# Performance work log

Hardware: AMD Instinct MI355X
Metric: run time of the kernel (lower is better)

## Reference

```python
import jax, jax.numpy as jnp
import numpy as np

B, P, M, C = 8192, 8, 2048, 1024


def setup_inputs() -> dict:
    key = jax.random.key(0)
    k1, k2 = jax.random.split(key)
    stdv = 1.0 / np.sqrt(C)
    inp = jax.random.normal(k1, (B, C), dtype=jnp.float32)
    weight = jax.random.uniform(k2, (P, M, C), dtype=jnp.float32, minval=-stdv, maxval=stdv)
    return {"input": inp, "weight": weight}


def reference(input, weight):
    # scores: [B, P, M] = <input_c, weight_pmc>
    att = jnp.einsum('bc,pmc->bpm', input, weight)
    att = jax.nn.softmax(att, axis=2)
    # combine with the same memory bank as values: [B, P, C]
    out = jnp.einsum('bpm,pmc->bpc', att, weight)
    return out
```

## Files before the change

### kernel.cpp

```cpp
#include <hip/hip_runtime.h>
#include <hip/hip_bf16.h>
#include <cstdint>
#include <cstddef>

#define B_SZ 8192
#define P_SZ 8
#define M_SZ 2048
#define C_SZ 1024

using bfrag = __attribute__((ext_vector_type(8))) short;
using facc  = __attribute__((ext_vector_type(4))) float;
using u16x4 = __attribute__((ext_vector_type(4))) unsigned short;

typedef __attribute__((address_space(1))) const void g_void;
typedef __attribute__((address_space(3))) void l_void;

__device__ __forceinline__ unsigned short f2bf(float x) {
    union { __hip_bfloat16 h; unsigned short u; } cv;
    cv.h = __float2bfloat16(x);
    return cv.u;
}
__device__ __forceinline__ float bf2f(unsigned short u) {
    union { unsigned int i; float f; } cv;
    cv.i = ((unsigned int)u) << 16;
    return cv.f;
}

#define WAIT_LGKM0() do { asm volatile("s_waitcnt lgkmcnt(0)" ::: "memory"); \
                          __builtin_amdgcn_sched_barrier(0); } while (0)
#define WAIT_VM(n)   do { asm volatile("s_waitcnt vmcnt(" #n ")" ::: "memory"); \
                          __builtin_amdgcn_sched_barrier(0); } while (0)
#define S_BARRIER()     asm volatile("s_barrier" ::: "memory")
#define LGKM0_BARRIER() asm volatile("s_waitcnt lgkmcnt(0)\n\ts_barrier" ::: "memory")
#define WAIT_VM_RAW(n)  asm volatile("s_waitcnt vmcnt(" #n ")" ::: "memory")

__global__ void cvt_q_kernel(const float* __restrict__ in, unsigned short* __restrict__ q) {
    const size_t i = (size_t)blockIdx.x * blockDim.x + threadIdx.x;
    const float4 v = ((const float4*)in)[i];
    u16x4 o = { f2bf(v.x), f2bf(v.y), f2bf(v.z), f2bf(v.w) };
    ((u16x4*)q)[i] = o;
}

__global__ void cvt_w_kernel(const float* __restrict__ w,
                             unsigned short* __restrict__ wb,
                             unsigned short* __restrict__ wt) {
    __shared__ float t[32][33];
    const int bid = blockIdx.x;
    const int p  = bid >> 11;
    const int m0 = ((bid >> 5) & 63) << 5;
    const int c0 = (bid & 31) << 5;
    const int tx = threadIdx.x & 7;
    const int ty = threadIdx.x >> 3;
    const float4 v = *(const float4*)(w + ((size_t)p*M_SZ + m0 + ty)*C_SZ + c0 + tx*4);
    u16x4 o = { f2bf(v.x), f2bf(v.y), f2bf(v.z), f2bf(v.w) };
    *(u16x4*)(wb + ((size_t)p*M_SZ + m0 + ty)*C_SZ + c0 + tx*4) = o;
    t[ty][tx*4+0] = v.x; t[ty][tx*4+1] = v.y; t[ty][tx*4+2] = v.z; t[ty][tx*4+3] = v.w;
    __syncthreads();
    float4 u2;
    u2.x = t[tx*4+0][ty]; u2.y = t[tx*4+1][ty]; u2.z = t[tx*4+2][ty]; u2.w = t[tx*4+3][ty];
    u16x4 o2 = { f2bf(u2.x), f2bf(u2.y), f2bf(u2.z), f2bf(u2.w) };
    *(u16x4*)(wt + ((size_t)p*C_SZ + c0 + ty)*M_SZ + m0 + tx*4) = o2;
}

constexpr int GLDS = 131072;

template<int KLEN>
__device__ __forceinline__ void stage_half8(const unsigned short* panelBase, char* ldsOp,
                                            int hh, int kt, int tid) {
    #pragma unroll
    for (int i = 0; i < 2; ++i) {
        const int o  = i*8192 + tid*16;
        const int rl = o >> 7;
        const int r  = hh*128 + rl;
        const int ps = (o >> 4) & 7;
        const int ls = ps ^ (r & 7);
        const unsigned short* src = panelBase + (size_t)r*KLEN + kt*64 + ls*8;
        char* dst = ldsOp + hh*16384 + i*8192 + ((tid >> 6) << 10);
        __builtin_amdgcn_global_load_lds((g_void*)src, (l_void*)dst, 16, 0, 0);
    }
}

__device__ __forceinline__ void loadA8(const char* ldsAbuf, int qm, int wm, int l15, int g,
                                       bfrag (&aF)[4][2]) {
    #pragma unroll
    for (int mf = 0; mf < 4; ++mf) {
        const int r = qm*128 + wm*64 + mf*16 + l15;
        const char* rp = ldsAbuf + r*128;
        #pragma unroll
        for (int ks = 0; ks < 2; ++ks)
            aF[mf][ks] = *(const bfrag*)(rp + (((ks*4 + g) ^ (r & 7)) << 4));
    }
}

__device__ __forceinline__ void loadB8(const char* ldsBbuf, int qn, int wn, int l15, int g,
                                       bfrag (&bF)[2][2]) {
    #pragma unroll
    for (int nf = 0; nf < 2; ++nf) {
        const int r = qn*128 + wn*32 + nf*16 + l15;
        const char* rp = ldsBbuf + r*128;
        #pragma unroll
        for (int ks = 0; ks < 2; ++ks)
            bF[nf][ks] = *(const bfrag*)(rp + (((ks*4 + g) ^ (r & 7)) << 4));
    }
}

template<int QM, int QN, int MODE, int DOSUM>
__device__ __forceinline__ void mfma_phase(const bfrag (&aF)[4][2], const bfrag (&bF)[2][2],
                                           facc (&acc)[8][4], float (&rs)[8]) {
    __builtin_amdgcn_s_setprio(1);
    #pragma unroll
    for (int ks = 0; ks < 2; ++ks)
        #pragma unroll
        for (int mf = 0; mf < 4; ++mf)
            #pragma unroll
            for (int nf = 0; nf < 2; ++nf)
                acc[QM*4 + mf][QN*2 + nf] = __builtin_amdgcn_mfma_f32_16x16x32_bf16(
                    aF[mf][ks], bF[nf][ks], acc[QM*4 + mf][QN*2 + nf], 0, 0, 0);
    if (MODE == 1 && DOSUM) {
        #pragma unroll
        for (int mf = 0; mf < 4; ++mf)
            #pragma unroll
            for (int ks = 0; ks < 2; ++ks)
                #pragma unroll
                for (int e = 0; e < 8; ++e)
                    rs[QM*4 + mf] += bf2f((unsigned short)aF[mf][ks][e]);
    }
    __builtin_amdgcn_s_setprio(0);
}

template<int KLEN, int NTN, int MODE>
__global__ __launch_bounds__(512, 2)
void gemm8(const unsigned short* __restrict__ A,
           const unsigned short* __restrict__ Bm,
           unsigned short* __restrict__ Pout,
           float* __restrict__ Oout,
           size_t APS, size_t BPS)
{
    extern __shared__ char lds[];
    const int tid  = threadIdx.x;
    const int lane = tid & 63;
    const int wid  = tid >> 6;
    const int wm   = wid >> 2;
    const int wn   = wid & 3;
    const int g    = lane >> 4;
    const int l15  = lane & 15;

    const int p       = blockIdx.x & 7;
    const int logical = blockIdx.x >> 3;
    const int nt      = logical % NTN;
    const int mt      = logical / NTN;

    const unsigned short* Abase = A  + (size_t)p*APS + (size_t)mt*256*KLEN;
    const unsigned short* Bbase = Bm + (size_t)p*BPS + (size_t)nt*256*KLEN;

    facc acc[8][4];
    #pragma unroll
    for (int i = 0; i < 8; ++i)
        #pragma unroll
        for (int j = 0; j < 4; ++j) acc[i][j] = facc{0.f, 0.f, 0.f, 0.f};
    float rs[8] = {0.f,0.f,0.f,0.f,0.f,0.f,0.f,0.f};

    constexpr int NKT = KLEN / 64;

    stage_half8<KLEN>(Bbase, lds + 32768,         0, 0, tid);
    stage_half8<KLEN>(Abase, lds + 0,             0, 0, tid);
    stage_half8<KLEN>(Bbase, lds + 32768,         1, 0, tid);
    stage_half8<KLEN>(Abase, lds + 0,             1, 0, tid);
    stage_half8<KLEN>(Abase, lds + 65536,         0, (1 < NKT ? 1 : NKT-1), tid);
    stage_half8<KLEN>(Bbase, lds + 65536 + 32768, 1, (1 < NKT ? 1 : NKT-1), tid);
    WAIT_VM(4);
    __builtin_amdgcn_s_barrier();

    bfrag aF[4][2], bLow[2][2], bHigh[2][2];

    for (int t = 0; t < NKT; ++t) {
        const int cur = t & 1;
        char* ldsA  = lds + cur*65536;
        char* ldsB  = ldsA + 32768;
        char* ldsAn = lds + (cur^1)*65536;
        char* ldsBn = ldsAn + 32768;
        const int t1 = (t+1 < NKT) ? t+1 : NKT-1;
        const int t2 = (t+2 < NKT) ? t+2 : NKT-1;

        loadA8(ldsA, 0, wm, l15, g, aF);
        loadB8(ldsB, 0, wn, l15, g, bLow);
        stage_half8<KLEN>(Bbase, ldsBn, 0, t1, tid);
        __builtin_amdgcn_s_barrier();
        WAIT_LGKM0();
        mfma_phase<0,0,MODE,1>(aF, bLow, acc, rs);
        __builtin_amdgcn_s_barrier();

        loadB8(ldsB, 1, wn, l15, g, bHigh);
        stage_half8<KLEN>(Abase, ldsAn, 1, t1, tid);
        __builtin_amdgcn_s_barrier();
        WAIT_LGKM0();
        mfma_phase<0,1,MODE,0>(aF, bHigh, acc, rs);
        __builtin_amdgcn_s_barrier();

        loadA8(ldsA, 1, wm, l15, g, aF);
        stage_half8<KLEN>(Abase, ldsA, 0, t2, tid);
        __builtin_amdgcn_s_barrier();
        WAIT_LGKM0();
        mfma_phase<1,1,MODE,1>(aF, bHigh, acc, rs);
        __builtin_amdgcn_s_barrier();

        stage_half8<KLEN>(Bbase, ldsB, 1, t2, tid);
        __builtin_amdgcn_s_barrier();
        mfma_phase<1,0,MODE,0>(aF, bLow, acc, rs);
        WAIT_VM(4);
        __builtin_amdgcn_s_barrier();
    }

    const int row0g = mt*256;
    const int col0g = nt*256;
    if (MODE == 0) {
        unsigned short* Pp = Pout + (size_t)p * ((size_t)B_SZ * M_SZ);
        #pragma unroll
        for (int qm = 0; qm < 2; ++qm)
            #pragma unroll
            for (int mf = 0; mf < 4; ++mf)
                #pragma unroll
                for (int j = 0; j < 4; ++j) {
                    const int r = row0g + qm*128 + wm*64 + mf*16 + g*4 + j;
                    unsigned short* rp = Pp + (size_t)r*M_SZ + col0g + wn*32 + l15;
                    #pragma unroll
                    for (int qn = 0; qn < 2; ++qn)
                        #pragma unroll
                        for (int nf = 0; nf < 2; ++nf)
                            rp[qn*128 + nf*16] = f2bf(__expf(acc[qm*4+mf][qn*2+nf][j]));
                }
    } else {
        #pragma unroll
        for (int qm = 0; qm < 2; ++qm)
            #pragma unroll
            for (int mf = 0; mf < 4; ++mf) {
                float d = rs[qm*4 + mf];
                d += __shfl_xor(d, 16);
                d += __shfl_xor(d, 32);
                #pragma unroll
                for (int j = 0; j < 4; ++j) {
                    const float inv = 1.0f / __shfl(d, g*4 + j);
                    const int r = row0g + qm*128 + wm*64 + mf*16 + g*4 + j;
                    float* op = Oout + ((size_t)r*P_SZ + p)*C_SZ + col0g + wn*32 + l15;
                    #pragma unroll
                    for (int qn = 0; qn < 2; ++qn)
                        #pragma unroll
                        for (int nf = 0; nf < 2; ++nf)
                            op[qn*128 + nf*16] = acc[qm*4+mf][qn*2+nf][j] * inv;
                }
            }
    }
}

template<int KLEN, int NTN, int CPX, int MODE>
__global__ __launch_bounds__(256, 2)
void gemm_tile(const unsigned short* __restrict__ A,
               const unsigned short* __restrict__ Bm,
               unsigned short* __restrict__ Pout,
               float* __restrict__ Oout,
               int p)
{
    __shared__ alignas(16) char lds[32768];
    const int tid  = threadIdx.x;
    const int lane = tid & 63;
    const int wid  = tid >> 6;
    const int wr   = wid >> 1;
    const int wc   = wid & 1;
    const int g    = lane >> 4;
    const int l15  = lane & 15;

    const int logical = (blockIdx.x & 7) * CPX + (blockIdx.x >> 3);
    const int mt = logical / NTN;
    const int nt = logical % NTN;

    const unsigned short* Abase = A  + (size_t)mt * 128 * KLEN;
    const unsigned short* Bbase = Bm + (size_t)nt * 128 * KLEN;

    facc acc[4][4];
    #pragma unroll
    for (int i = 0; i < 4; ++i)
        #pragma unroll
        for (int j = 0; j < 4; ++j) acc[i][j] = facc{0.f, 0.f, 0.f, 0.f};
    float rs[4] = {0.f, 0.f, 0.f, 0.f};

    constexpr int NKT = KLEN / 32;

    auto stage = [&](int kt) {
        char* buf = lds + (kt & 1) * 16384;
        const unsigned short* As = Abase + kt * 32;
        const unsigned short* Bs = Bbase + kt * 32;
        #pragma unroll
        for (int i = 0; i < 2; ++i) {
            const int o  = i * 4096 + tid * 16;
            const int r  = o >> 6;
            const int s  = (o >> 4) & 3;
            const int cs = s ^ ((r >> 1) & 3);
            __builtin_amdgcn_global_load_lds((g_void*)(As + (size_t)r * KLEN + cs * 8),
                                             (l_void*)(buf + i * 4096 + ((tid >> 6) << 10)),
                                             16, 0, 0);
        }
        #pragma unroll
        for (int i = 0; i < 2; ++i) {
            const int o  = i * 4096 + tid * 16;
            const int r  = o >> 6;
            const int s  = (o >> 4) & 3;
            const int cs = s ^ ((r >> 1) & 3);
            __builtin_amdgcn_global_load_lds((g_void*)(Bs + (size_t)r * KLEN + cs * 8),
                                             (l_void*)(buf + 8192 + i * 4096 + ((tid >> 6) << 10)),
                                             16, 0, 0);
        }
    };

    stage(0);
    stage(1);

    const int cb = ((((l15 >> 1) & 3) ^ g) << 4);

    for (int kt = 0; kt < NKT; ++kt) {
        if (kt + 1 < NKT) { WAIT_VM_RAW(4); } else { WAIT_VM_RAW(0); }
        S_BARRIER();
        const char* Ab = lds + (kt & 1) * 16384;
        const char* Bb = Ab + 8192;
        bfrag af[4], bb[4];
        #pragma unroll
        for (int mf = 0; mf < 4; ++mf)
            af[mf] = *(const bfrag*)(Ab + (wr * 64 + mf * 16 + l15) * 64 + cb);
        #pragma unroll
        for (int nf = 0; nf < 4; ++nf)
            bb[nf] = *(const bfrag*)(Bb + (wc * 64 + nf * 16 + l15) * 64 + cb);
        LGKM0_BARRIER();
        if (kt + 2 < NKT) stage(kt + 2);
        if (MODE == 1) {
            #pragma unroll
            for (int mf = 0; mf < 4; ++mf)
                #pragma unroll
                for (int e = 0; e < 8; ++e)
                    rs[mf] += bf2f((unsigned short)af[mf][e]);
        }
        #pragma unroll
        for (int mf = 0; mf < 4; ++mf)
            #pragma unroll
            for (int nf = 0; nf < 4; ++nf)
                acc[mf][nf] = __builtin_amdgcn_mfma_f32_16x16x32_bf16(af[mf], bb[nf], acc[mf][nf], 0, 0, 0);
    }

    if (MODE == 0) {
        const int prow0 = mt * 128 + wr * 64;
        const int pcol0 = nt * 128 + wc * 64;
        #pragma unroll
        for (int mf = 0; mf < 4; ++mf)
            #pragma unroll
            for (int j = 0; j < 4; ++j) {
                const size_t rbase = (size_t)(prow0 + mf * 16 + g * 4 + j) * M_SZ + pcol0 + l15;
                #pragma unroll
                for (int nf = 0; nf < 4; ++nf)
                    Pout[rbase + nf * 16] = f2bf(__expf(acc[mf][nf][j]));
            }
    } else {
        const int orow0 = mt * 128 + wr * 64;
        const int ocol0 = nt * 128 + wc * 64;
        #pragma unroll
        for (int mf = 0; mf < 4; ++mf) {
            float d = rs[mf];
            d += __shfl_xor(d, 16);
            d += __shfl_xor(d, 32);
            #pragma unroll
            for (int j = 0; j < 4; ++j) {
                const float inv = 1.0f / __shfl(d, g * 4 + j);
                const size_t rbase = ((size_t)(orow0 + mf * 16 + g * 4 + j) * P_SZ + p) * C_SZ
                                   + ocol0 + l15;
                #pragma unroll
                for (int nf = 0; nf < 4; ++nf)
                    Oout[rbase + nf * 16] = acc[mf][nf][j] * inv;
            }
        }
    }
}

__global__ void emu_fallback(const float* __restrict__ inF, const float* __restrict__ wF,
                             float* __restrict__ out)
{
    __shared__ float sc[M_SZ];
    __shared__ float qs[C_SZ];
    __shared__ float wsum[4];
    const int b = blockIdx.x;
    const int tid = threadIdx.x;
    for (int c = tid; c < C_SZ; c += 256) qs[c] = inF[(size_t)b*C_SZ + c];
    __syncthreads();
    for (int p = 0; p < P_SZ; ++p) {
        const float* wp = wF + (size_t)p*M_SZ*C_SZ;
        for (int m = tid; m < M_SZ; m += 256) {
            float d = 0.f;
            const float* wr = wp + (size_t)m*C_SZ;
            for (int c = 0; c < C_SZ; ++c) d += qs[c]*wr[c];
            sc[m] = __expf(d);
        }
        __syncthreads();
        float part = 0.f;
        for (int m = tid; m < M_SZ; m += 256) part += sc[m];
        #pragma unroll
        for (int sft = 1; sft < 64; sft <<= 1) part += __shfl_xor(part, sft);
        if ((tid & 63) == 0) wsum[tid >> 6] = part;
        __syncthreads();
        const float rin = 1.0f / (wsum[0] + wsum[1] + wsum[2] + wsum[3]);
        float o0=0,o1=0,o2=0,o3=0;
        for (int m = 0; m < M_SZ; ++m) {
            const float pm = sc[m];
            const float4 w4 = *(const float4*)(wp + (size_t)m*C_SZ + tid*4);
            o0 += pm*w4.x; o1 += pm*w4.y; o2 += pm*w4.z; o3 += pm*w4.w;
        }
        float* op = out + ((size_t)b*P_SZ + p)*C_SZ + tid*4;
        op[0]=o0*rin; op[1]=o1*rin; op[2]=o2*rin; op[3]=o3*rin;
        __syncthreads();
    }
}

extern "C" void kernel_launch(void* const* d_in, const int* in_sizes, int n_in,
                              void* d_out, int out_size, void* d_ws, size_t ws_size,
                              hipStream_t stream)
{
    (void)in_sizes; (void)n_in; (void)out_size;
    const float* inF = (const float*)d_in[0];
    const float* wF  = (const float*)d_in[1];
    float* out = (float*)d_out;

    const size_t wbE  = (size_t)P_SZ * M_SZ * C_SZ;
    const size_t qE   = (size_t)B_SZ * C_SZ;
    const size_t pME  = (size_t)B_SZ * M_SZ;
    const size_t pAll = pME * P_SZ;
    const size_t needBig   = (wbE*2 + qE + pAll) * sizeof(unsigned short);
    const size_t needMid   = (wbE*2 + qE + pME)  * sizeof(unsigned short);

    if (ws_size >= needBig) {
        unsigned short* wb = (unsigned short*)d_ws;
        unsigned short* wt = wb + wbE;
        unsigned short* qb = wt + wbE;
        unsigned short* Pb = qb + qE;
        cvt_q_kernel<<<(unsigned)(qE/4/256), 256, 0, stream>>>(inF, qb);
        cvt_w_kernel<<<P_SZ*64*32, 256, 0, stream>>>(wF, wb, wt);
        hipFuncSetAttribute(reinterpret_cast<const void*>(&gemm8<C_SZ, 8, 0>),
                            hipFuncAttributeMaxDynamicSharedMemorySize, GLDS);
        gemm8<C_SZ, 8, 0><<<2048, 512, GLDS, stream>>>(
            qb, wb, Pb, nullptr, (size_t)0, (size_t)M_SZ * C_SZ);
        hipFuncSetAttribute(reinterpret_cast<const void*>(&gemm8<M_SZ, 4, 1>),
                            hipFuncAttributeMaxDynamicSharedMemorySize, GLDS);
        gemm8<M_SZ, 4, 1><<<1024, 512, GLDS, stream>>>(
            Pb, wt, nullptr, out, (size_t)B_SZ * M_SZ, (size_t)C_SZ * M_SZ);
    } else if (ws_size >= needMid) {
        unsigned short* wb = (unsigned short*)d_ws;
        unsigned short* wt = wb + wbE;
        unsigned short* qb = wt + wbE;
        unsigned short* Pb = qb + qE;
        cvt_q_kernel<<<(unsigned)(qE/4/256), 256, 0, stream>>>(inF, qb);
        cvt_w_kernel<<<P_SZ*64*32, 256, 0, stream>>>(wF, wb, wt);
        for (int p = 0; p < P_SZ; ++p) {
            gemm_tile<C_SZ, 16, 128, 0><<<1024, 256, 0, stream>>>(
                qb, wb + (size_t)p*M_SZ*C_SZ, Pb, nullptr, p);
            gemm_tile<M_SZ, 8, 64, 1><<<512, 256, 0, stream>>>(
                Pb, wt + (size_t)p*C_SZ*M_SZ, nullptr, out, p);
        }
    } else {
        emu_fallback<<<B_SZ, 256, 0, stream>>>(inF, wF, out);
    }
}
```

Before: 640.8 us.

## Process two N-subtiles per block with a continuous K pipeline across subtiles

Each block of both GEMM kernels now computes two consecutive 256-wide output tiles. The K-loop runs over both subtiles as one flattened sequence, so staging of the next subtile's B data overlaps the current subtile's tail and epilogue. Accumulators are written out and reset at each subtile boundary. This halves the grid and amortizes pipeline prologue and drain, at the cost of fewer blocks (possible load imbalance on 256 CUs) and an epilogue placed inside the main loop.

```diff
diff --git a/kernel.cpp b/kernel.cpp
--- a/kernel.cpp
+++ b/kernel.cpp
@@ -128,7 +128,7 @@
     __builtin_amdgcn_s_setprio(0);
 }
 
-template<int KLEN, int NTN, int MODE>
+template<int KLEN, int NTNO, int MODE, int SUBT>
 __global__ __launch_bounds__(512, 2)
 void gemm8(const unsigned short* __restrict__ A,
            const unsigned short* __restrict__ Bm,
@@ -147,11 +147,11 @@
 
     const int p       = blockIdx.x & 7;
     const int logical = blockIdx.x >> 3;
-    const int nt      = logical % NTN;
-    const int mt      = logical / NTN;
-
-    const unsigned short* Abase = A  + (size_t)p*APS + (size_t)mt*256*KLEN;
-    const unsigned short* Bbase = Bm + (size_t)p*BPS + (size_t)nt*256*KLEN;
+    const int nt_o    = logical % NTNO;
+    const int mt      = logical / NTNO;
+
+    const unsigned short* Abase  = A  + (size_t)p*APS + (size_t)mt*256*KLEN;
+    const unsigned short* Bbase0 = Bm + (size_t)p*BPS + (size_t)nt_o*SUBT*256*KLEN;
 
     facc acc[8][4];
     #pragma unroll
@@ -161,94 +161,108 @@
     float rs[8] = {0.f,0.f,0.f,0.f,0.f,0.f,0.f,0.f};
 
     constexpr int NKT = KLEN / 64;
-
-    stage_half8<KLEN>(Bbase, lds + 32768,         0, 0, tid);
-    stage_half8<KLEN>(Abase, lds + 0,             0, 0, tid);
-    stage_half8<KLEN>(Bbase, lds + 32768,         1, 0, tid);
-    stage_half8<KLEN>(Abase, lds + 0,             1, 0, tid);
-    stage_half8<KLEN>(Abase, lds + 65536,         0, (1 < NKT ? 1 : NKT-1), tid);
-    stage_half8<KLEN>(Bbase, lds + 65536 + 32768, 1, (1 < NKT ? 1 : NKT-1), tid);
+    constexpr int T   = NKT * SUBT;
+
+    stage_half8<KLEN>(Bbase0, lds + 32768,         0, 0, tid);
+    stage_half8<KLEN>(Abase,  lds + 0,             0, 0, tid);
+    stage_half8<KLEN>(Bbase0, lds + 32768,         1, 0, tid);
+    stage_half8<KLEN>(Abase,  lds + 0,             1, 0, tid);
+    stage_half8<KLEN>(Abase,  lds + 65536,         0, 1, tid);
+    stage_half8<KLEN>(Bbase0, lds + 65536 + 32768, 1, 1, tid);
     WAIT_VM(4);
     __builtin_amdgcn_s_barrier();
 
     bfrag aF[4][2], bLow[2][2], bHigh[2][2];
 
-    for (int t = 0; t < NKT; ++t) {
-        const int cur = t & 1;
+    for (int tau = 0; tau < T; ++tau) {
+        const int cur = tau & 1;
         char* ldsA  = lds + cur*65536;
         char* ldsB  = ldsA + 32768;
         char* ldsAn = lds + (cur^1)*65536;
         char* ldsBn = ldsAn + 32768;
-        const int t1 = (t+1 < NKT) ? t+1 : NKT-1;
-        const int t2 = (t+2 < NKT) ? t+2 : NKT-1;
+        const int t1 = (tau+1 < T) ? tau+1 : T-1;
+        const int t2 = (tau+2 < T) ? tau+2 : T-1;
+        const int k1 = t1 & (NKT-1), s1 = t1 / NKT;
+        const int k2 = t2 & (NKT-1), s2 = t2 / NKT;
+        const unsigned short* B1b = Bbase0 + (size_t)s1*256*KLEN;
+        const unsigned short* B2b = Bbase0 + (size_t)s2*256*KLEN;
 
         loadA8(ldsA, 0, wm, l15, g, aF);
         loadB8(ldsB, 0, wn, l15, g, bLow);
-        stage_half8<KLEN>(Bbase, ldsBn, 0, t1, tid);
+        stage_half8<KLEN>(B1b, ldsBn, 0, k1, tid);
         __builtin_amdgcn_s_barrier();
         WAIT_LGKM0();
         mfma_phase<0,0,MODE,1>(aF, bLow, acc, rs);
         __builtin_amdgcn_s_barrier();
 
         loadB8(ldsB, 1, wn, l15, g, bHigh);
-        stage_half8<KLEN>(Abase, ldsAn, 1, t1, tid);
+        stage_half8<KLEN>(Abase, ldsAn, 1, k1, tid);
         __builtin_amdgcn_s_barrier();
         WAIT_LGKM0();
         mfma_phase<0,1,MODE,0>(aF, bHigh, acc, rs);
         __builtin_amdgcn_s_barrier();
 
         loadA8(ldsA, 1, wm, l15, g, aF);
-        stage_half8<KLEN>(Abase, ldsA, 0, t2, tid);
+        stage_half8<KLEN>(Abase, ldsA, 0, k2, tid);
         __builtin_amdgcn_s_barrier();
         WAIT_LGKM0();
         mfma_phase<1,1,MODE,1>(aF, bHigh, acc, rs);
         __builtin_amdgcn_s_barrier();
 
-        stage_half8<KLEN>(Bbase, ldsB, 1, t2, tid);
+        stage_half8<KLEN>(B2b, ldsB, 1, k2, tid);
         __builtin_amdgcn_s_barrier();
         mfma_phase<1,0,MODE,0>(aF, bLow, acc, rs);
         WAIT_VM(4);
         __builtin_amdgcn_s_barrier();
-    }
-
-    const int row0g = mt*256;
-    const int col0g = nt*256;
-    if (MODE == 0) {
-        unsigned short* Pp = Pout + (size_t)p * ((size_t)B_SZ * M_SZ);
-        #pragma unroll
-        for (int qm = 0; qm < 2; ++qm)
-            #pragma unroll
-            for (int mf = 0; mf < 4; ++mf)
-                #pragma unroll
-                for (int j = 0; j < 4; ++j) {
-                    const int r = row0g + qm*128 + wm*64 + mf*16 + g*4 + j;
-                    unsigned short* rp = Pp + (size_t)r*M_SZ + col0g + wn*32 + l15;
+
+        if ((tau & (NKT-1)) == NKT-1) {
+            const int sub   = tau / NKT;
+            const int row0g = mt*256;
+            const int col0g = (nt_o*SUBT + sub)*256;
+            if (MODE == 0) {
+                unsigned short* Pp = Pout + (size_t)p * ((size_t)B_SZ * M_SZ);
+                #pragma unroll
+                for (int qm = 0; qm < 2; ++qm)
                     #pragma unroll
-                    for (int qn = 0; qn < 2; ++qn)
+                    for (int mf = 0; mf < 4; ++mf)
                         #pragma unroll
-                        for (int nf = 0; nf < 2; ++nf)
-                            rp[qn*128 + nf*16] = f2bf(__expf(acc[qm*4+mf][qn*2+nf][j]));
-                }
-    } else {
-        #pragma unroll
-        for (int qm = 0; qm < 2; ++qm)
-            #pragma unroll
-            for (int mf = 0; mf < 4; ++mf) {
-                float d = rs[qm*4 + mf];
-                d += __shfl_xor(d, 16);
-                d += __shfl_xor(d, 32);
-                #pragma unroll
-                for (int j = 0; j < 4; ++j) {
-                    const float inv = 1.0f / __shfl(d, g*4 + j);
-                    const int r = row0g + qm*128 + wm*64 + mf*16 + g*4 + j;
-                    float* op = Oout + ((size_t)r*P_SZ + p)*C_SZ + col0g + wn*32 + l15;
+                        for (int j = 0; j < 4; ++j) {
+                            const int r = row0g + qm*128 + wm*64 + mf*16 + g*4 + j;
+                            unsigned short* rp = Pp + (size_t)r*M_SZ + col0g + wn*32 + l15;
+                            #pragma unroll
+                            for (int qn = 0; qn < 2; ++qn)
+                                #pragma unroll
+                                for (int nf = 0; nf < 2; ++nf)
+                                    rp[qn*128 + nf*16] = f2bf(__expf(acc[qm*4+mf][qn*2+nf][j]));
+                        }
+            } else {
+                #pragma unroll
+                for (int qm = 0; qm < 2; ++qm)
                     #pragma unroll
-                    for (int qn = 0; qn < 2; ++qn)
+                    for (int mf = 0; mf < 4; ++mf) {
+                        float d = rs[qm*4 + mf];
+                        d += __shfl_xor(d, 16);
+                        d += __shfl_xor(d, 32);
                         #pragma unroll
-                        for (int nf = 0; nf < 2; ++nf)
-                            op[qn*128 + nf*16] = acc[qm*4+mf][qn*2+nf][j] * inv;
-                }
+                        for (int j = 0; j < 4; ++j) {
+                            const float inv = 1.0f / __shfl(d, g*4 + j);
+                            const int r = row0g + qm*128 + wm*64 + mf*16 + g*4 + j;
+                            float* op = Oout + ((size_t)r*P_SZ + p)*C_SZ + col0g + wn*32 + l15;
+                            #pragma unroll
+                            for (int qn = 0; qn < 2; ++qn)
+                                #pragma unroll
+                                for (int nf = 0; nf < 2; ++nf)
+                                    op[qn*128 + nf*16] = acc[qm*4+mf][qn*2+nf][j] * inv;
+                        }
+                    }
             }
+            #pragma unroll
+            for (int i = 0; i < 8; ++i)
+                #pragma unroll
+                for (int j = 0; j < 4; ++j) acc[i][j] = facc{0.f, 0.f, 0.f, 0.f};
+            #pragma unroll
+            for (int i = 0; i < 8; ++i) rs[i] = 0.f;
+        }
     }
 }
 
@@ -438,13 +452,13 @@
         unsigned short* Pb = qb + qE;
         cvt_q_kernel<<<(unsigned)(qE/4/256), 256, 0, stream>>>(inF, qb);
         cvt_w_kernel<<<P_SZ*64*32, 256, 0, stream>>>(wF, wb, wt);
-        hipFuncSetAttribute(reinterpret_cast<const void*>(&gemm8<C_SZ, 8, 0>),
+        hipFuncSetAttribute(reinterpret_cast<const void*>(&gemm8<C_SZ, 4, 0, 2>),
                             hipFuncAttributeMaxDynamicSharedMemorySize, GLDS);
-        gemm8<C_SZ, 8, 0><<<2048, 512, GLDS, stream>>>(
+        gemm8<C_SZ, 4, 0, 2><<<1024, 512, GLDS, stream>>>(
             qb, wb, Pb, nullptr, (size_t)0, (size_t)M_SZ * C_SZ);
-        hipFuncSetAttribute(reinterpret_cast<const void*>(&gemm8<M_SZ, 4, 1>),
+        hipFuncSetAttribute(reinterpret_cast<const void*>(&gemm8<M_SZ, 2, 1, 2>),
                             hipFuncAttributeMaxDynamicSharedMemorySize, GLDS);
-        gemm8<M_SZ, 4, 1><<<1024, 512, GLDS, stream>>>(
+        gemm8<M_SZ, 2, 1, 2><<<512, 512, GLDS, stream>>>(
             Pb, wt, nullptr, out, (size_t)B_SZ * M_SZ, (size_t)C_SZ * M_SZ);
     } else if (ws_size >= needMid) {
         unsigned short* wb = (unsigned short*)d_ws;
```

Result: slower. 712.7 us (+11.2%).

## Load B operand directly from global in first GEMM, staging only A in LDS

Applied to the files above, without the earlier changes.

Adds a variant of the score GEMM that stages only the shared input tile A through LDS (double-buffered, 64KB) and has each wave read its weight B fragments straight from global memory into registers. The goal is to halve LDS footprint and staging traffic, possibly enabling more overlap, while relying on cache for B reuse. The tradeoff is that direct global B loads are uncoalesced row-strided reads that go through L2 latency inside the inner loop, and every wave group rereads them.

```diff
diff --git a/kernel.cpp b/kernel.cpp
--- a/kernel.cpp
+++ b/kernel.cpp
@@ -62,7 +62,8 @@
     *(u16x4*)(wt + ((size_t)p*C_SZ + c0 + ty)*M_SZ + m0 + tx*4) = o2;
 }
 
-constexpr int GLDS = 131072;
+constexpr int GLDS  = 131072;
+constexpr int GLDS1 = 65536;
 
 template<int KLEN>
 __device__ __forceinline__ void stage_half8(const unsigned short* panelBase, char* ldsOp,
@@ -104,6 +105,18 @@
     }
 }
 
+template<int KLEN>
+__device__ __forceinline__ void loadBdir(const unsigned short* Bb, int qn, int wn, int l15, int g,
+                                         int kt, bfrag (&bF)[2][2]) {
+    #pragma unroll
+    for (int nf = 0; nf < 2; ++nf) {
+        const unsigned short* rp = Bb + (size_t)(qn*128 + wn*32 + nf*16 + l15)*KLEN
+                                 + kt*64 + g*8;
+        bF[nf][0] = *(const bfrag*)(rp);
+        bF[nf][1] = *(const bfrag*)(rp + 32);
+    }
+}
+
 template<int QM, int QN, int MODE, int DOSUM>
 __device__ __forceinline__ void mfma_phase(const bfrag (&aF)[4][2], const bfrag (&bF)[2][2],
                                            facc (&acc)[8][4], float (&rs)[8]) {
@@ -126,6 +139,96 @@
                     rs[QM*4 + mf] += bf2f((unsigned short)aF[mf][ks][e]);
     }
     __builtin_amdgcn_s_setprio(0);
+}
+
+template<int KLEN, int NTN>
+__global__ __launch_bounds__(512, 2)
+void gemm1bd(const unsigned short* __restrict__ A,
+             const unsigned short* __restrict__ Bm,
+             unsigned short* __restrict__ Pout,
+             size_t APS, size_t BPS)
+{
+    extern __shared__ char lds[];
+    const int tid  = threadIdx.x;
+    const int lane = tid & 63;
+    const int wid  = tid >> 6;
+    const int wm   = wid >> 2;
+    const int wn   = wid & 3;
+    const int g    = lane >> 4;
+    const int l15  = lane & 15;
+
+    const int p       = blockIdx.x & 7;
+    const int logical = blockIdx.x >> 3;
+    const int nt      = logical % NTN;
+    const int mt      = logical / NTN;
+
+    const unsigned short* Abase = A  + (size_t)p*APS + (size_t)mt*256*KLEN;
+    const unsigned short* Bbase = Bm + (size_t)p*BPS + (size_t)nt*256*KLEN;
+
+    facc acc[8][4];
+    #pragma unroll
+    for (int i = 0; i < 8; ++i)
+        #pragma unroll
+        for (int j = 0; j < 4; ++j) acc[i][j] = facc{0.f, 0.f, 0.f, 0.f};
+    float rs[8];
+
+    constexpr int NKT = KLEN / 64;
+
+    stage_half8<KLEN>(Abase, lds, 0, 0, tid);
+    stage_half8<KLEN>(Abase, lds, 1, 0, tid);
+    WAIT_VM(0);
+    __builtin_amdgcn_s_barrier();
+
+    bfrag aF[4][2], bLow[2][2], bHigh[2][2];
+
+    for (int t = 0; t < NKT; ++t) {
+        const int cur = t & 1;
+        char* ldsA  = lds + cur*32768;
+        char* ldsAn = lds + (cur^1)*32768;
+        const int k1 = (t+1 < NKT) ? t+1 : NKT-1;
+
+        loadBdir<KLEN>(Bbase, 0, wn, l15, g, t, bLow);
+        loadBdir<KLEN>(Bbase, 1, wn, l15, g, t, bHigh);
+        loadA8(ldsA, 0, wm, l15, g, aF);
+        stage_half8<KLEN>(Abase, ldsAn, 0, k1, tid);
+        __builtin_amdgcn_s_barrier();
+        WAIT_LGKM0();
+        mfma_phase<0,0,0,0>(aF, bLow, acc, rs);
+        __builtin_amdgcn_s_barrier();
+
+        loadA8(ldsA, 1, wm, l15, g, aF);
+        stage_half8<KLEN>(Abase, ldsAn, 1, k1, tid);
+        __builtin_amdgcn_s_barrier();
+        WAIT_LGKM0();
+        mfma_phase<1,0,0,0>(aF, bLow, acc, rs);
+        __builtin_amdgcn_s_barrier();
+
+        mfma_phase<1,1,0,0>(aF, bHigh, acc, rs);
+
+        loadA8(ldsA, 0, wm, l15, g, aF);
+        WAIT_LGKM0();
+        mfma_phase<0,1,0,0>(aF, bHigh, acc, rs);
+        WAIT_VM(0);
+        __builtin_amdgcn_s_barrier();
+    }
+
+    const int row0g = mt*256;
+    const int col0g = nt*256;
+    unsigned short* Pp = Pout + (size_t)p * ((size_t)B_SZ * M_SZ);
+    #pragma unroll
+    for (int qm = 0; qm < 2; ++qm)
+        #pragma unroll
+        for (int mf = 0; mf < 4; ++mf)
+            #pragma unroll
+            for (int j = 0; j < 4; ++j) {
+                const int r = row0g + qm*128 + wm*64 + mf*16 + g*4 + j;
+                unsigned short* rp = Pp + (size_t)r*M_SZ + col0g + wn*32 + l15;
+                #pragma unroll
+                for (int qn = 0; qn < 2; ++qn)
+                    #pragma unroll
+                    for (int nf = 0; nf < 2; ++nf)
+                        rp[qn*128 + nf*16] = f2bf(__expf(acc[qm*4+mf][qn*2+nf][j]));
+            }
 }
 
 template<int KLEN, int NTN, int MODE>
@@ -438,10 +541,10 @@
         unsigned short* Pb = qb + qE;
         cvt_q_kernel<<<(unsigned)(qE/4/256), 256, 0, stream>>>(inF, qb);
         cvt_w_kernel<<<P_SZ*64*32, 256, 0, stream>>>(wF, wb, wt);
-        hipFuncSetAttribute(reinterpret_cast<const void*>(&gemm8<C_SZ, 8, 0>),
-                            hipFuncAttributeMaxDynamicSharedMemorySize, GLDS);
-        gemm8<C_SZ, 8, 0><<<2048, 512, GLDS, stream>>>(
-            qb, wb, Pb, nullptr, (size_t)0, (size_t)M_SZ * C_SZ);
+        hipFuncSetAttribute(reinterpret_cast<const void*>(&gemm1bd<C_SZ, 8>),
+                            hipFuncAttributeMaxDynamicSharedMemorySize, GLDS1);
+        gemm1bd<C_SZ, 8><<<2048, 512, GLDS1, stream>>>(
+            qb, wb, Pb, (size_t)0, (size_t)M_SZ * C_SZ);
         hipFuncSetAttribute(reinterpret_cast<const void*>(&gemm8<M_SZ, 4, 1>),
                             hipFuncAttributeMaxDynamicSharedMemorySize, GLDS);
         gemm8<M_SZ, 4, 1><<<1024, 512, GLDS, stream>>>(
```

After: 825.1 us. +28.8%, slower.

## Restructure GEMM main loop into a two-barrier pipeline with split A fragments

Applied to the files above, without the earlier changes.

Reworks the per-tile loop of the bf16 GEMM kernel. Separate low and high A fragment registers allow LDS reads to be issued earlier and waited on with partial lgkmcnt counts instead of full drains. Most block-wide barriers are removed, cutting them from eight per K-tile to two. This aims to overlap LDS loads and global staging with MFMA work, at the cost of higher register pressure and more delicate hazard ordering between staged writes and reads.

```diff
diff --git a/kernel.cpp b/kernel.cpp
--- a/kernel.cpp
+++ b/kernel.cpp
@@ -26,10 +26,11 @@
     return cv.f;
 }
 
-#define WAIT_LGKM0() do { asm volatile("s_waitcnt lgkmcnt(0)" ::: "memory"); \
+#define WAIT_LGKM(n) do { asm volatile("s_waitcnt lgkmcnt(" #n ")" ::: "memory"); \
                           __builtin_amdgcn_sched_barrier(0); } while (0)
 #define WAIT_VM(n)   do { asm volatile("s_waitcnt vmcnt(" #n ")" ::: "memory"); \
                           __builtin_amdgcn_sched_barrier(0); } while (0)
+#define SFENCE()     __builtin_amdgcn_sched_barrier(0)
 #define S_BARRIER()     asm volatile("s_barrier" ::: "memory")
 #define LGKM0_BARRIER() asm volatile("s_waitcnt lgkmcnt(0)\n\ts_barrier" ::: "memory")
 #define WAIT_VM_RAW(n)  asm volatile("s_waitcnt vmcnt(" #n ")" ::: "memory")
@@ -130,7 +131,7 @@
 
 template<int KLEN, int NTN, int MODE>
 __global__ __launch_bounds__(512, 2)
-void gemm8(const unsigned short* __restrict__ A,
+void gemm9(const unsigned short* __restrict__ A,
            const unsigned short* __restrict__ Bm,
            unsigned short* __restrict__ Pout,
            float* __restrict__ Oout,
@@ -166,12 +167,12 @@
     stage_half8<KLEN>(Abase, lds + 0,             0, 0, tid);
     stage_half8<KLEN>(Bbase, lds + 32768,         1, 0, tid);
     stage_half8<KLEN>(Abase, lds + 0,             1, 0, tid);
-    stage_half8<KLEN>(Abase, lds + 65536,         0, (1 < NKT ? 1 : NKT-1), tid);
-    stage_half8<KLEN>(Bbase, lds + 65536 + 32768, 1, (1 < NKT ? 1 : NKT-1), tid);
+    stage_half8<KLEN>(Abase, lds + 65536,         0, 1, tid);
+    stage_half8<KLEN>(Bbase, lds + 65536 + 32768, 1, 1, tid);
     WAIT_VM(4);
     __builtin_amdgcn_s_barrier();
 
-    bfrag aF[4][2], bLow[2][2], bHigh[2][2];
+    bfrag aLow[4][2], aHigh[4][2], bLow[2][2], bHigh[2][2];
 
     for (int t = 0; t < NKT; ++t) {
         const int cur = t & 1;
@@ -179,34 +180,36 @@
         char* ldsB  = ldsA + 32768;
         char* ldsAn = lds + (cur^1)*65536;
         char* ldsBn = ldsAn + 32768;
-        const int t1 = (t+1 < NKT) ? t+1 : NKT-1;
-        const int t2 = (t+2 < NKT) ? t+2 : NKT-1;
-
-        loadA8(ldsA, 0, wm, l15, g, aF);
+        const int k1 = (t+1 < NKT) ? t+1 : NKT-1;
+        const int k2 = (t+2 < NKT) ? t+2 : NKT-1;
+
         loadB8(ldsB, 0, wn, l15, g, bLow);
-        stage_half8<KLEN>(Bbase, ldsBn, 0, t1, tid);
+        loadA8(ldsA, 0, wm, l15, g, aLow);
+        SFENCE();
+        loadB8(ldsB, 1, wn, l15, g, bHigh);
+        SFENCE();
+        stage_half8<KLEN>(Bbase, ldsBn, 0, k1, tid);
+        stage_half8<KLEN>(Abase, ldsAn, 1, k1, tid);
+        SFENCE();
+
+        WAIT_LGKM(4);
+        mfma_phase<0,0,MODE,1>(aLow, bLow, acc, rs);
+
+        loadA8(ldsA, 1, wm, l15, g, aHigh);
+        SFENCE();
+        WAIT_LGKM(8);
+        mfma_phase<0,1,MODE,0>(aLow, bHigh, acc, rs);
+
         __builtin_amdgcn_s_barrier();
-        WAIT_LGKM0();
-        mfma_phase<0,0,MODE,1>(aF, bLow, acc, rs);
-        __builtin_amdgcn_s_barrier();
-
-        loadB8(ldsB, 1, wn, l15, g, bHigh);
-        stage_half8<KLEN>(Abase, ldsAn, 1, t1, tid);
-        __builtin_amdgcn_s_barrier();
-        WAIT_LGKM0();
-        mfma_phase<0,1,MODE,0>(aF, bHigh, acc, rs);
-        __builtin_amdgcn_s_barrier();
-
-        loadA8(ldsA, 1, wm, l15, g, aF);
-        stage_half8<KLEN>(Abase, ldsA, 0, t2, tid);
-        __builtin_amdgcn_s_barrier();
-        WAIT_LGKM0();
-        mfma_phase<1,1,MODE,1>(aF, bHigh, acc, rs);
-        __builtin_amdgcn_s_barrier();
-
-        stage_half8<KLEN>(Bbase, ldsB, 1, t2, tid);
-        __builtin_amdgcn_s_barrier();
-        mfma_phase<1,0,MODE,0>(aF, bLow, acc, rs);
+
+        stage_half8<KLEN>(Abase, ldsA, 0, k2, tid);
+        stage_half8<KLEN>(Bbase, ldsB, 1, k2, tid);
+        SFENCE();
+
+        WAIT_LGKM(0);
+        mfma_phase<1,1,MODE,1>(aHigh, bHigh, acc, rs);
+        mfma_phase<1,0,MODE,0>(aHigh, bLow, acc, rs);
+
         WAIT_VM(4);
         __builtin_amdgcn_s_barrier();
     }
@@ -438,13 +441,13 @@
         unsigned short* Pb = qb + qE;
         cvt_q_kernel<<<(unsigned)(qE/4/256), 256, 0, stream>>>(inF, qb);
         cvt_w_kernel<<<P_SZ*64*32, 256, 0, stream>>>(wF, wb, wt);
-        hipFuncSetAttribute(reinterpret_cast<const void*>(&gemm8<C_SZ, 8, 0>),
+        hipFuncSetAttribute(reinterpret_cast<const void*>(&gemm9<C_SZ, 8, 0>),
                             hipFuncAttributeMaxDynamicSharedMemorySize, GLDS);
-        gemm8<C_SZ, 8, 0><<<2048, 512, GLDS, stream>>>(
+        gemm9<C_SZ, 8, 0><<<2048, 512, GLDS, stream>>>(
             qb, wb, Pb, nullptr, (size_t)0, (size_t)M_SZ * C_SZ);
-        hipFuncSetAttribute(reinterpret_cast<const void*>(&gemm8<M_SZ, 4, 1>),
+        hipFuncSetAttribute(reinterpret_cast<const void*>(&gemm9<M_SZ, 4, 1>),
                             hipFuncAttributeMaxDynamicSharedMemorySize, GLDS);
-        gemm8<M_SZ, 4, 1><<<1024, 512, GLDS, stream>>>(
+        gemm9<M_SZ, 4, 1><<<1024, 512, GLDS, stream>>>(
             Pb, wt, nullptr, out, (size_t)B_SZ * M_SZ, (size_t)C_SZ * M_SZ);
     } else if (ws_size >= needMid) {
         unsigned short* wb = (unsigned short*)d_ws;
```

Result: slower. 662.8 us (+3.4%).
